# Optimization experiments

Measured on AMD Instinct MI355X. Metric: run time of the kernel, lower is better.

The kernel has to match this reference:

```python
import jax, jax.numpy as jnp
import numpy as np

BASE = 7.0
TWO_PI = 2.0 * np.pi
MAX_PATHS = 9

def _mod_phase(x):
    # ModularPhaseNorm(hidden, base=7): periodic phase nonlinearity
    return jnp.sin(TWO_PI * x / BASE)

def _branch(data, W):
    # data: [N, F, P], W: [O, F] -> [N, O, 3P] with per-path (neg, zero, pos) branches
    pos = jnp.einsum('nfp,of->nop', data, W)
    n, o, p = pos.shape
    tri = jnp.stack([-pos, jnp.zeros_like(pos), pos], axis=-1)  # [N,O,P,3]
    return tri.reshape(n, o, p * 3)

def _scorer(data, w1, b1, w2, b2):
    # data: [N, F, P] -> scores [N, P]  (linear -> modular phase -> linear)
    z = _mod_phase(jnp.einsum('nfp,hf->nph', data, w1) + b1)
    return (jnp.einsum('nph,oh->npo', z, w2) + b2)[..., 0]

def _prune(data, weights):
    # keep top-k paths by softmax weight, renormalize kept weights
    w_k, idx = jax.lax.top_k(weights, MAX_PATHS)
    data_k = jnp.take_along_axis(data, idx[:, None, :], axis=2)
    w_k = w_k / jnp.clip(jnp.sum(w_k, axis=1, keepdims=True), 1e-8)
    return data_k, w_k

def _forward(x, W1, W2, Wout, s1a_w, s1a_b, s1b_w, s1b_b, s2a_w, s2a_b, s2b_w, s2b_b, soa_w, soa_b, sob_w, sob_b):
    batch, choices, dims = x.shape
    data = x.reshape(batch * choices, dims)[:, :, None]  # 1 path
    weights = None
    for W, aw, ab, bw, bb in ((W1, s1a_w, s1a_b, s1b_w, s1b_b),
                              (W2, s2a_w, s2a_b, s2b_w, s2b_b)):
        data = jnp.tanh(_branch(data, W))
        weights = jax.nn.softmax(_scorer(data, aw, ab, bw, bb), axis=1)
        if data.shape[2] > MAX_PATHS:  # static shape condition
            data, weights = _prune(data, weights)
    data = _branch(data, Wout)  # [N, 1, 27]
    weights = jax.nn.softmax(_scorer(data, soa_w, soa_b, sob_w, sob_b), axis=1)
    if data.shape[2] > MAX_PATHS:
        data, weights = _prune(data, weights)
    out = jnp.sum(data * weights[:, None, :], axis=2)  # weighted collapse -> [N, 1]
    return out.reshape(batch, choices)

def setup_inputs():
    key = jax.random.key(0)
    ks = jax.random.split(key, 12)
    B, C, D, H, SH, SHO = 64, 64, 1024, 1024, 64, 32
    def lin(k, o, i):
        return jax.random.normal(k, (o, i), jnp.float32) / np.sqrt(i)
    return {
        'x': jax.random.normal(ks[0], (B, C, D), jnp.float32),
        'W1': lin(ks[1], H, D),
        'W2': lin(ks[2], H, H),
        'Wout': lin(ks[3], 1, H),
        's1a_w': lin(ks[4], SH, H), 's1a_b': jnp.zeros((SH,), jnp.float32),
        's1b_w': lin(ks[5], 1, SH), 's1b_b': jnp.zeros((1,), jnp.float32),
        's2a_w': lin(ks[6], SH, H), 's2a_b': jnp.zeros((SH,), jnp.float32),
        's2b_w': lin(ks[7], 1, SH), 's2b_b': jnp.zeros((1,), jnp.float32),
        'soa_w': lin(ks[8], SHO, 1), 'soa_b': jnp.zeros((SHO,), jnp.float32),
        'sob_w': lin(ks[9], 1, SHO), 'sob_b': jnp.zeros((1,), jnp.float32),
    }

def reference(x, W1, W2, Wout, s1a_w, s1a_b, s1b_w, s1b_b, s2a_w, s2a_b, s2b_w, s2b_b, soa_w, soa_b, sob_w, sob_b):
    return _forward(x, W1, W2, Wout, s1a_w, s1a_b, s1b_w, s1b_b, s2a_w, s2a_b, s2b_w, s2b_b, soa_w, soa_b, sob_w, sob_b)
```

## Files before the change

kernel.cpp:

```cpp
#include <hip/hip_runtime.h>


typedef __attribute__((ext_vector_type(4))) float     f32x4;
typedef __attribute__((ext_vector_type(8))) _Float16  f16x8;

#define AS1 __attribute__((address_space(1)))
#define AS3 __attribute__((address_space(3)))
#define GLOAD16(gp, lp) \
    __builtin_amdgcn_global_load_lds((AS1 const void*)(gp), (AS3 void*)(lp), 16, 0, 0)

__global__ __launch_bounds__(256)
void pbcs_cvt(const float* __restrict__ x,  _Float16* __restrict__ xo,
              const float* __restrict__ w1, _Float16* __restrict__ w1o,
              const float* __restrict__ w2, _Float16* __restrict__ w2o)
{
    const int b = blockIdx.x;
    const float* src; _Float16* dst; int idx;
    if (b < 2048)      { src = x;  dst = xo;  idx = b * 256 + threadIdx.x; }
    else if (b < 2560) { src = w1; dst = w1o; idx = (b - 2048) * 256 + threadIdx.x; }
    else               { src = w2; dst = w2o; idx = (b - 2560) * 256 + threadIdx.x; }
    const float4 v0 = ((const float4*)src)[idx * 2];
    const float4 v1 = ((const float4*)src)[idx * 2 + 1];
    f16x8 h;
    h[0] = (_Float16)v0.x; h[1] = (_Float16)v0.y;
    h[2] = (_Float16)v0.z; h[3] = (_Float16)v0.w;
    h[4] = (_Float16)v1.x; h[5] = (_Float16)v1.y;
    h[6] = (_Float16)v1.z; h[7] = (_Float16)v1.w;
    ((f16x8*)dst)[idx] = h;
}

template<int EPI>
__global__ __launch_bounds__(256, 2)
void pbcs_gemm16(const _Float16* __restrict__ A, const _Float16* __restrict__ B,
                 _Float16* __restrict__ Cout, const float* __restrict__ wout,
                 float* __restrict__ s_part)
{
    __shared__ char smem[2][32768];

    const int tid  = threadIdx.x;
    const int lane = tid & 63;
    const int wid  = tid >> 6;
    const int wm   = wid >> 1;
    const int wn   = wid & 1;
    const int l15  = lane & 15;
    const int g    = lane >> 4;

    const int b  = blockIdx.x;
    const int bm = (b & 7) * 4 + ((b >> 3) & 3);
    const int bn = b >> 5;

    const char* aS[4]; const char* bS[4]; int aD[4], bD[4];
#pragma unroll
    for (int j = 0; j < 4; ++j) {
        const int c = wid * 4 + j;
        const int r = c * 8 + (lane >> 3), s = lane & 7;
        aS[j] = (const char*)A + (size_t)(bm * 128 + r) * 2048 + 16 * (s ^ (r & 7));
        aD[j] = c * 1024;
        bS[j] = (const char*)B + (size_t)(bn * 128 + r) * 2048 + 16 * (s ^ (r & 7));
        bD[j] = 16384 + c * 1024;
    }

    int aoff[4][2], boff[4][2];
#pragma unroll
    for (int f = 0; f < 4; ++f) {
        const int ra = wm * 64 + f * 16 + l15;
        const int rb = wn * 64 + f * 16 + l15;
#pragma unroll
        for (int kh = 0; kh < 2; ++kh) {
            aoff[f][kh] = ra * 128 + 16 * (((kh << 2) | g) ^ (ra & 7));
            boff[f][kh] = 16384 + rb * 128 + 16 * (((kh << 2) | g) ^ (rb & 7));
        }
    }

    f32x4 acc[4][4];
#pragma unroll
    for (int i = 0; i < 4; ++i)
#pragma unroll
        for (int j = 0; j < 4; ++j) acc[i][j] = (f32x4)0.f;

#define STAGE(buf, kt) do {                                      \
        const int _ko = (kt) * 128;                              \
        _Pragma("unroll")                                        \
        for (int _j = 0; _j < 4; ++_j) {                         \
            GLOAD16(aS[_j] + _ko, smem[buf] + aD[_j]);           \
            GLOAD16(bS[_j] + _ko, smem[buf] + bD[_j]);           \
        }                                                        \
    } while (0)

#define COMPUTE(buf) do {                                                        \
        _Pragma("unroll")                                                        \
        for (int _kh = 0; _kh < 2; ++_kh) {                                      \
            f16x8 _a[4], _b[4];                                                  \
            _Pragma("unroll")                                                    \
            for (int _f = 0; _f < 4; ++_f) {                                     \
                _a[_f] = *(const f16x8*)(smem[buf] + aoff[_f][_kh]);             \
                _b[_f] = *(const f16x8*)(smem[buf] + boff[_f][_kh]);             \
            }                                                                    \
            _Pragma("unroll")                                                    \
            for (int _mf = 0; _mf < 4; ++_mf)                                    \
            _Pragma("unroll")                                                    \
            for (int _nf = 0; _nf < 4; ++_nf)                                    \
                acc[_mf][_nf] = __builtin_amdgcn_mfma_f32_16x16x32_f16(          \
                    _a[_mf], _b[_nf], acc[_mf][_nf], 0, 0, 0);                   \
        }                                                                        \
    } while (0)

    STAGE(0, 0);
    STAGE(1, 1);
#pragma unroll 1
    for (int t = 0; t < 15; ++t) {
        asm volatile("s_waitcnt vmcnt(8)" ::: "memory");
        __builtin_amdgcn_s_barrier();
        __builtin_amdgcn_sched_barrier(0);
        COMPUTE(t & 1);
        asm volatile("s_waitcnt lgkmcnt(0)" ::: "memory");
        __builtin_amdgcn_sched_barrier(0);
        __builtin_amdgcn_s_barrier();
        if (t < 14) STAGE(t & 1, t + 2);
    }
    asm volatile("s_waitcnt vmcnt(0)" ::: "memory");
    __builtin_amdgcn_s_barrier();
    __builtin_amdgcn_sched_barrier(0);
    COMPUTE(1);

    if (EPI == 0) {
#pragma unroll
        for (int mf = 0; mf < 4; ++mf)
#pragma unroll
        for (int nf = 0; nf < 4; ++nf)
#pragma unroll
        for (int jj = 0; jj < 4; ++jj) {
            const int row = bm * 128 + wm * 64 + mf * 16 + g * 4 + jj;
            const int col = bn * 128 + wn * 64 + nf * 16 + l15;
            Cout[(size_t)row * 1024 + col] = (_Float16)tanhf(acc[mf][nf][jj]);
        }
    } else {
        float w[4];
#pragma unroll
        for (int nf = 0; nf < 4; ++nf)
            w[nf] = wout[bn * 128 + wn * 64 + nf * 16 + l15];
#pragma unroll
        for (int mf = 0; mf < 4; ++mf)
#pragma unroll
        for (int jj = 0; jj < 4; ++jj) {
            float v = 0.f;
#pragma unroll
            for (int nf = 0; nf < 4; ++nf)
                v += tanhf(acc[mf][nf][jj]) * w[nf];
            v += __shfl_xor(v, 1, 64);
            v += __shfl_xor(v, 2, 64);
            v += __shfl_xor(v, 4, 64);
            v += __shfl_xor(v, 8, 64);
            if (l15 == 0) {
                const int row = bm * 128 + wm * 64 + mf * 16 + g * 4 + jj;
                s_part[row * 16 + bn * 2 + wn] = v;
            }
        }
    }
#undef STAGE
#undef COMPUTE
}

__global__ __launch_bounds__(256)
void pbcs_finalize(const float* __restrict__ s_part,
                   const float* __restrict__ soa_w, const float* __restrict__ soa_b,
                   const float* __restrict__ sob_w, const float* __restrict__ sob_b,
                   float* __restrict__ out, int Nrows)
{
    const int row  = blockIdx.x * 4 + (threadIdx.x >> 6);
    const int lane = threadIdx.x & 63;
    if (row >= Nrows) return;

    float part = (lane < 16) ? s_part[row * 16 + lane] : 0.f;
#pragma unroll
    for (int off = 32; off > 0; off >>= 1) part += __shfl_xor(part, off, 64);
    const float s = part;

    const float C7 = 0.8975979010256552f;
    float tS = 0.f, tZ = 0.f, tN = 0.f;
    if (lane < 32) {
        const float aw = soa_w[lane];
        const float ab = soa_b[lane];
        const float bw = sob_w[lane];
        tS = bw * sinf(C7 * fmaf(aw,  s, ab));
        tZ = bw * sinf(C7 * ab);
        tN = bw * sinf(C7 * fmaf(aw, -s, ab));
    }
#pragma unroll
    for (int off = 32; off > 0; off >>= 1) {
        tS += __shfl_xor(tS, off, 64);
        tZ += __shfl_xor(tZ, off, 64);
        tN += __shfl_xor(tN, off, 64);
    }
    const float bb = sob_b[0];
    const float fS = tS + bb;
    const float f0 = tZ + bb;
    const float fN = tN + bb;

    const int j  = lane;
    const int kk = j / 3;
    const int q  = j - kk * 3;
    const int p  = ((0x101 >> kk) & 1) - ((0x044 >> kk) & 1);
    const int c  = (q == 0) ? -p : ((q == 2) ? p : 0);
    const float val = (float)c * s;
    const float sc  = (c == 0) ? f0 : ((c > 0) ? fS : fN);

    int rank = 0;
#pragma unroll 1
    for (int i = 0; i < 27; ++i) {
        const float sci = __shfl(sc, i, 64);
        rank += (sci > sc) || (sci == sc && i < j);
    }
    const float mx = fmaxf(fS, fmaxf(f0, fN));
    float e = (j < 27 && rank < 9) ? expf(sc - mx) : 0.f;
    float num = val * e;
    float den = e;
#pragma unroll
    for (int off = 32; off > 0; off >>= 1) {
        num += __shfl_xor(num, off, 64);
        den += __shfl_xor(den, off, 64);
    }
    if (lane == 0) out[row] = num / den;
}

extern "C" void kernel_launch(void* const* d_in, const int* in_sizes, int n_in,
                              void* d_out, int out_size, void* d_ws, size_t ws_size,
                              hipStream_t stream)
{
    const float* x     = (const float*)d_in[0];
    const float* W1    = (const float*)d_in[1];
    const float* W2    = (const float*)d_in[2];
    const float* Wout  = (const float*)d_in[3];
    const float* soa_w = (const float*)d_in[12];
    const float* soa_b = (const float*)d_in[13];
    const float* sob_w = (const float*)d_in[14];
    const float* sob_b = (const float*)d_in[15];

    const int Nr = 4096;
    char* ws = (char*)d_ws;
    _Float16* xf  = (_Float16*)ws;
    _Float16* t1f = (_Float16*)(ws + (8u  << 20));
    _Float16* w1f = (_Float16*)(ws + (16u << 20));
    _Float16* w2f = (_Float16*)(ws + (18u << 20));
    float* s_part = (float*)(ws + (20u << 20));

    pbcs_cvt<<<3072, 256, 0, stream>>>(x, xf, W1, w1f, W2, w2f);

    pbcs_gemm16<0><<<256, 256, 0, stream>>>(xf,  w1f, t1f, nullptr, nullptr);
    pbcs_gemm16<1><<<256, 256, 0, stream>>>(t1f, w2f, nullptr, Wout, s_part);

    pbcs_finalize<<<Nr / 4, 256, 0, stream>>>(s_part, soa_w, soa_b, sob_w, sob_b,
                                              (float*)d_out, Nr);
}
```

Measured before the change: 56.30 us.

## Retile GEMMs to 64x128 blocks of two waves with triple-buffered LDS

Changes the two fp16 MFMA GEMMs from 128x128 tiles with four waves to 64x128 tiles with two waves, doubling the grid to 512 blocks. Shared memory becomes a three-stage ring of 24KB buffers, and the wait allows more loads in flight. The block-to-tile mapping is also reworked so consecutive blocks spread across XCDs. The aim is to fill more CUs on the 256-CU part and hide more load latency, at the cost of less data reuse per block and more global/L2 traffic.

```diff
diff --git a/kernel.cpp b/kernel.cpp
--- a/kernel.cpp
+++ b/kernel.cpp
@@ -30,45 +30,51 @@
 }
 
 template<int EPI>
-__global__ __launch_bounds__(256, 2)
+__global__ __launch_bounds__(128)
 void pbcs_gemm16(const _Float16* __restrict__ A, const _Float16* __restrict__ B,
                  _Float16* __restrict__ Cout, const float* __restrict__ wout,
                  float* __restrict__ s_part)
 {
-    __shared__ char smem[2][32768];
+    __shared__ char smem[3][24576];
 
     const int tid  = threadIdx.x;
     const int lane = tid & 63;
     const int wid  = tid >> 6;
-    const int wm   = wid >> 1;
-    const int wn   = wid & 1;
     const int l15  = lane & 15;
     const int g    = lane >> 4;
 
     const int b  = blockIdx.x;
-    const int bm = (b & 7) * 4 + ((b >> 3) & 3);
-    const int bn = b >> 5;
-
-    const char* aS[4]; const char* bS[4]; int aD[4], bD[4];
-#pragma unroll
-    for (int j = 0; j < 4; ++j) {
-        const int c = wid * 4 + j;
-        const int r = c * 8 + (lane >> 3), s = lane & 7;
-        aS[j] = (const char*)A + (size_t)(bm * 128 + r) * 2048 + 16 * (s ^ (r & 7));
-        aD[j] = c * 1024;
-        bS[j] = (const char*)B + (size_t)(bn * 128 + r) * 2048 + 16 * (s ^ (r & 7));
-        bD[j] = 16384 + c * 1024;
-    }
+    const int id = (b & 7) * 64 + (b >> 3);
+    const int bm = id >> 3;
+    const int bn = id & 7;
+
+    const int r = lane >> 3, s = lane & 7;
+    const char* aBase = (const char*)A
+        + (size_t)(bm * 64 + wid * 8 + r) * 2048 + 16 * (s ^ r);
+    const char* bBase = (const char*)B
+        + (size_t)(bn * 128 + wid * 8 + r) * 2048 + 16 * (s ^ r);
+
+#define STAGE(buf, kt) do {                                                   \
+        const int _ko = (kt) * 128;                                           \
+        _Pragma("unroll")                                                     \
+        for (int _j = 0; _j < 4; ++_j)               \
+            GLOAD16(aBase + _j * (16 * 2048) + _ko,                           \
+                    smem[buf] + (2 * _j + wid) * 1024);                       \
+        _Pragma("unroll")                                                     \
+        for (int _j = 0; _j < 8; ++_j)               \
+            GLOAD16(bBase + _j * (16 * 2048) + _ko,                           \
+                    smem[buf] + 8192 + (2 * _j + wid) * 1024);                \
+    } while (0)
 
     int aoff[4][2], boff[4][2];
 #pragma unroll
     for (int f = 0; f < 4; ++f) {
-        const int ra = wm * 64 + f * 16 + l15;
-        const int rb = wn * 64 + f * 16 + l15;
+        const int ra = f * 16 + l15;
+        const int rb = wid * 64 + f * 16 + l15;
 #pragma unroll
         for (int kh = 0; kh < 2; ++kh) {
             aoff[f][kh] = ra * 128 + 16 * (((kh << 2) | g) ^ (ra & 7));
-            boff[f][kh] = 16384 + rb * 128 + 16 * (((kh << 2) | g) ^ (rb & 7));
+            boff[f][kh] = 8192 + rb * 128 + 16 * (((kh << 2) | g) ^ (rb & 7));
         }
     }
 
@@ -77,15 +83,6 @@
     for (int i = 0; i < 4; ++i)
 #pragma unroll
         for (int j = 0; j < 4; ++j) acc[i][j] = (f32x4)0.f;
-
-#define STAGE(buf, kt) do {                                      \
-        const int _ko = (kt) * 128;                              \
-        _Pragma("unroll")                                        \
-        for (int _j = 0; _j < 4; ++_j) {                         \
-            GLOAD16(aS[_j] + _ko, smem[buf] + aD[_j]);           \
-            GLOAD16(bS[_j] + _ko, smem[buf] + bD[_j]);           \
-        }                                                        \
-    } while (0)
 
 #define COMPUTE(buf) do {                                                        \
         _Pragma("unroll")                                                        \
@@ -107,21 +104,24 @@
 
     STAGE(0, 0);
     STAGE(1, 1);
+    int cb = 0, sb = 2;
 #pragma unroll 1
     for (int t = 0; t < 15; ++t) {
-        asm volatile("s_waitcnt vmcnt(8)" ::: "memory");
+        asm volatile("s_waitcnt vmcnt(12)" ::: "memory");
         __builtin_amdgcn_s_barrier();
         __builtin_amdgcn_sched_barrier(0);
-        COMPUTE(t & 1);
+        COMPUTE(cb);
         asm volatile("s_waitcnt lgkmcnt(0)" ::: "memory");
         __builtin_amdgcn_sched_barrier(0);
         __builtin_amdgcn_s_barrier();
-        if (t < 14) STAGE(t & 1, t + 2);
+        if (t < 14) STAGE(sb, t + 2);
+        cb = (cb == 2) ? 0 : cb + 1;
+        sb = (sb == 2) ? 0 : sb + 1;
     }
     asm volatile("s_waitcnt vmcnt(0)" ::: "memory");
     __builtin_amdgcn_s_barrier();
     __builtin_amdgcn_sched_barrier(0);
-    COMPUTE(1);
+    COMPUTE(0);
 
     if (EPI == 0) {
 #pragma unroll
@@ -130,15 +130,15 @@
         for (int nf = 0; nf < 4; ++nf)
 #pragma unroll
         for (int jj = 0; jj < 4; ++jj) {
-            const int row = bm * 128 + wm * 64 + mf * 16 + g * 4 + jj;
-            const int col = bn * 128 + wn * 64 + nf * 16 + l15;
+            const int row = bm * 64 + mf * 16 + g * 4 + jj;
+            const int col = bn * 128 + wid * 64 + nf * 16 + l15;
             Cout[(size_t)row * 1024 + col] = (_Float16)tanhf(acc[mf][nf][jj]);
         }
     } else {
         float w[4];
 #pragma unroll
         for (int nf = 0; nf < 4; ++nf)
-            w[nf] = wout[bn * 128 + wn * 64 + nf * 16 + l15];
+            w[nf] = wout[bn * 128 + wid * 64 + nf * 16 + l15];
 #pragma unroll
         for (int mf = 0; mf < 4; ++mf)
 #pragma unroll
@@ -152,8 +152,8 @@
             v += __shfl_xor(v, 4, 64);
             v += __shfl_xor(v, 8, 64);
             if (l15 == 0) {
-                const int row = bm * 128 + wm * 64 + mf * 16 + g * 4 + jj;
-                s_part[row * 16 + bn * 2 + wn] = v;
+                const int row = bm * 64 + mf * 16 + g * 4 + jj;
+                s_part[row * 16 + bn * 2 + wid] = v;
             }
         }
     }
@@ -246,8 +246,8 @@
 
     pbcs_cvt<<<3072, 256, 0, stream>>>(x, xf, W1, w1f, W2, w2f);
 
-    pbcs_gemm16<0><<<256, 256, 0, stream>>>(xf,  w1f, t1f, nullptr, nullptr);
-    pbcs_gemm16<1><<<256, 256, 0, stream>>>(t1f, w2f, nullptr, Wout, s_part);
+    pbcs_gemm16<0><<<512, 128, 0, stream>>>(xf,  w1f, t1f, nullptr, nullptr);
+    pbcs_gemm16<1><<<512, 128, 0, stream>>>(t1f, w2f, nullptr, Wout, s_part);
 
     pbcs_finalize<<<Nr / 4, 256, 0, stream>>>(s_part, soa_w, soa_b, sob_w, sob_b,
                                               (float*)d_out, Nr);
```

New measurement: 66.54 us. 1.18x slower.

## Split GEMM K dimension across two wave groups with LDS reduction

Applied to the files above, without the earlier changes.

Doubles the GEMM block to 512 threads, where two groups of four waves each handle half of the K range, with 128KB of dynamic LDS. Each group stages and computes its own K half in 8 iterations instead of 16, and the partial accumulators are then summed through LDS before the epilogue. The aim is more waves in flight per CU and a shorter serial K loop for the 256-block grid, which likely leaves CUs underfilled. In exchange it adds an LDS round-trip for the reduction, needs more LDS per block, and drops to one block per CU.

```diff
diff --git a/kernel.cpp b/kernel.cpp
--- a/kernel.cpp
+++ b/kernel.cpp
@@ -30,17 +30,18 @@
 }
 
 template<int EPI>
-__global__ __launch_bounds__(256, 2)
+__global__ __launch_bounds__(512, 1)
 void pbcs_gemm16(const _Float16* __restrict__ A, const _Float16* __restrict__ B,
                  _Float16* __restrict__ Cout, const float* __restrict__ wout,
                  float* __restrict__ s_part)
 {
-    __shared__ char smem[2][32768];
+    extern __shared__ char smem[];
 
     const int tid  = threadIdx.x;
     const int lane = tid & 63;
     const int wid  = tid >> 6;
-    const int wm   = wid >> 1;
+    const int wk   = wid >> 2;
+    const int wm   = (wid >> 1) & 1;
     const int wn   = wid & 1;
     const int l15  = lane & 15;
     const int g    = lane >> 4;
@@ -49,16 +50,25 @@
     const int bm = (b & 7) * 4 + ((b >> 3) & 3);
     const int bn = b >> 5;
 
-    const char* aS[4]; const char* bS[4]; int aD[4], bD[4];
-#pragma unroll
-    for (int j = 0; j < 4; ++j) {
-        const int c = wid * 4 + j;
-        const int r = c * 8 + (lane >> 3), s = lane & 7;
-        aS[j] = (const char*)A + (size_t)(bm * 128 + r) * 2048 + 16 * (s ^ (r & 7));
-        aD[j] = c * 1024;
-        bS[j] = (const char*)B + (size_t)(bn * 128 + r) * 2048 + 16 * (s ^ (r & 7));
-        bD[j] = 16384 + c * 1024;
-    }
+    const int r = lane >> 3, sslot = lane & 7;
+    const int isB = (wid >> 1) & 1;
+    const char* stageSrc[8]; int stageDst[8];
+#pragma unroll
+    for (int j = 0; j < 8; ++j) {
+        const int cc  = (wid & 1) * 8 + j;
+        const int row = (isB ? bn : bm) * 128 + cc * 8 + r;
+        const char* base = (const char*)(isB ? B : A);
+        stageSrc[j] = base + (size_t)row * 2048 + wk * 1024 + 16 * (sslot ^ r);
+        stageDst[j] = wk * 32768 + isB * 16384 + cc * 1024;
+    }
+
+#define STAGE(buf, kt) do {                                              \
+        const int _ko = (kt) * 128;                                      \
+        _Pragma("unroll")                                                \
+        for (int _j = 0; _j < 8; ++_j)                                   \
+            GLOAD16(stageSrc[_j] + _ko,                                  \
+                    smem + (buf) * 65536 + stageDst[_j]);                \
+    } while (0)
 
     int aoff[4][2], boff[4][2];
 #pragma unroll
@@ -78,23 +88,15 @@
 #pragma unroll
         for (int j = 0; j < 4; ++j) acc[i][j] = (f32x4)0.f;
 
-#define STAGE(buf, kt) do {                                      \
-        const int _ko = (kt) * 128;                              \
-        _Pragma("unroll")                                        \
-        for (int _j = 0; _j < 4; ++_j) {                         \
-            GLOAD16(aS[_j] + _ko, smem[buf] + aD[_j]);           \
-            GLOAD16(bS[_j] + _ko, smem[buf] + bD[_j]);           \
-        }                                                        \
-    } while (0)
-
 #define COMPUTE(buf) do {                                                        \
+        const char* _L = smem + (buf) * 65536 + wk * 32768;                      \
         _Pragma("unroll")                                                        \
         for (int _kh = 0; _kh < 2; ++_kh) {                                      \
             f16x8 _a[4], _b[4];                                                  \
             _Pragma("unroll")                                                    \
             for (int _f = 0; _f < 4; ++_f) {                                     \
-                _a[_f] = *(const f16x8*)(smem[buf] + aoff[_f][_kh]);             \
-                _b[_f] = *(const f16x8*)(smem[buf] + boff[_f][_kh]);             \
+                _a[_f] = *(const f16x8*)(_L + aoff[_f][_kh]);                    \
+                _b[_f] = *(const f16x8*)(_L + boff[_f][_kh]);                    \
             }                                                                    \
             _Pragma("unroll")                                                    \
             for (int _mf = 0; _mf < 4; ++_mf)                                    \
@@ -108,20 +110,36 @@
     STAGE(0, 0);
     STAGE(1, 1);
 #pragma unroll 1
-    for (int t = 0; t < 15; ++t) {
-        asm volatile("s_waitcnt vmcnt(8)" ::: "memory");
+    for (int t = 0; t < 8; ++t) {
+        if (t < 7) { asm volatile("s_waitcnt vmcnt(8)" ::: "memory"); }
+        else       { asm volatile("s_waitcnt vmcnt(0)" ::: "memory"); }
         __builtin_amdgcn_s_barrier();
         __builtin_amdgcn_sched_barrier(0);
         COMPUTE(t & 1);
         asm volatile("s_waitcnt lgkmcnt(0)" ::: "memory");
         __builtin_amdgcn_sched_barrier(0);
         __builtin_amdgcn_s_barrier();
-        if (t < 14) STAGE(t & 1, t + 2);
-    }
-    asm volatile("s_waitcnt vmcnt(0)" ::: "memory");
+        if (t < 6) STAGE(t & 1, t + 2);
+    }
+
+    const int pair = wm * 2 + wn;
+    if (wk == 1) {
+#pragma unroll
+        for (int mf = 0; mf < 4; ++mf)
+#pragma unroll
+        for (int nf = 0; nf < 4; ++nf)
+            *(f32x4*)(smem + pair * 16384 + (mf * 4 + nf) * 1024 + lane * 16)
+                = acc[mf][nf];
+    }
+    asm volatile("s_waitcnt lgkmcnt(0)" ::: "memory");
     __builtin_amdgcn_s_barrier();
-    __builtin_amdgcn_sched_barrier(0);
-    COMPUTE(1);
+    if (wk == 1) return;
+#pragma unroll
+    for (int mf = 0; mf < 4; ++mf)
+#pragma unroll
+    for (int nf = 0; nf < 4; ++nf)
+        acc[mf][nf] += *(const f32x4*)(smem + pair * 16384
+                                       + (mf * 4 + nf) * 1024 + lane * 16);
 
     if (EPI == 0) {
 #pragma unroll
@@ -244,10 +262,15 @@
     _Float16* w2f = (_Float16*)(ws + (18u << 20));
     float* s_part = (float*)(ws + (20u << 20));
 
+    hipFuncSetAttribute((const void*)pbcs_gemm16<0>,
+                        hipFuncAttributeMaxDynamicSharedMemorySize, 131072);
+    hipFuncSetAttribute((const void*)pbcs_gemm16<1>,
+                        hipFuncAttributeMaxDynamicSharedMemorySize, 131072);
+
     pbcs_cvt<<<3072, 256, 0, stream>>>(x, xf, W1, w1f, W2, w2f);
 
-    pbcs_gemm16<0><<<256, 256, 0, stream>>>(xf,  w1f, t1f, nullptr, nullptr);
-    pbcs_gemm16<1><<<256, 256, 0, stream>>>(t1f, w2f, nullptr, Wout, s_part);
+    pbcs_gemm16<0><<<256, 512, 131072, stream>>>(xf,  w1f, t1f, nullptr, nullptr);
+    pbcs_gemm16<1><<<256, 512, 131072, stream>>>(t1f, w2f, nullptr, Wout, s_part);
 
     pbcs_finalize<<<Nr / 4, 256, 0, stream>>>(s_part, soa_w, soa_b, sob_w, sob_b,
                                               (float*)d_out, Nr);
```

Result: no change. 56.63 us (+0.6%).

## Fuse fp32-to-fp16 conversion of x into first GEMM's LDS load path

Applied to the files above, without the earlier changes.

The separate pass that converted the 16 MB fp32 input x to fp16 is removed. The first GEMM now streams fp32 x tiles directly into LDS and converts to fp16 in registers before the MFMA. This drops a full read and write of x through global memory. In exchange it doubles A-tile LDS traffic and uses 96 KB of dynamic shared memory, which limits the GEMM to one block per CU, so latency hiding may suffer.

```diff
diff --git a/kernel.cpp b/kernel.cpp
--- a/kernel.cpp
+++ b/kernel.cpp
@@ -10,15 +10,13 @@
     __builtin_amdgcn_global_load_lds((AS1 const void*)(gp), (AS3 void*)(lp), 16, 0, 0)
 
 __global__ __launch_bounds__(256)
-void pbcs_cvt(const float* __restrict__ x,  _Float16* __restrict__ xo,
-              const float* __restrict__ w1, _Float16* __restrict__ w1o,
-              const float* __restrict__ w2, _Float16* __restrict__ w2o)
+void pbcs_cvt_w(const float* __restrict__ w1, _Float16* __restrict__ w1o,
+                const float* __restrict__ w2, _Float16* __restrict__ w2o)
 {
     const int b = blockIdx.x;
     const float* src; _Float16* dst; int idx;
-    if (b < 2048)      { src = x;  dst = xo;  idx = b * 256 + threadIdx.x; }
-    else if (b < 2560) { src = w1; dst = w1o; idx = (b - 2048) * 256 + threadIdx.x; }
-    else               { src = w2; dst = w2o; idx = (b - 2560) * 256 + threadIdx.x; }
+    if (b < 512) { src = w1; dst = w1o; idx = b * 256 + threadIdx.x; }
+    else         { src = w2; dst = w2o; idx = (b - 512) * 256 + threadIdx.x; }
     const float4 v0 = ((const float4*)src)[idx * 2];
     const float4 v1 = ((const float4*)src)[idx * 2 + 1];
     f16x8 h;
@@ -29,13 +27,11 @@
     ((f16x8*)dst)[idx] = h;
 }
 
-template<int EPI>
-__global__ __launch_bounds__(256, 2)
-void pbcs_gemm16(const _Float16* __restrict__ A, const _Float16* __restrict__ B,
-                 _Float16* __restrict__ Cout, const float* __restrict__ wout,
-                 float* __restrict__ s_part)
-{
-    __shared__ char smem[2][32768];
+__global__ __launch_bounds__(256, 1)
+void pbcs_gemm_xf32(const float* __restrict__ A, const _Float16* __restrict__ B,
+                    _Float16* __restrict__ Cout)
+{
+    extern __shared__ char smem[];
 
     const int tid  = threadIdx.x;
     const int lane = tid & 63;
@@ -44,6 +40,130 @@
     const int wn   = wid & 1;
     const int l15  = lane & 15;
     const int g    = lane >> 4;
+    const int m7   = l15 & 7;
+
+    const int b  = blockIdx.x;
+    const int bm = (b & 7) * 4 + ((b >> 3) & 3);
+    const int bn = b >> 5;
+
+    const int r = lane >> 3, s = lane & 7;
+    const char* aS[8]; int aD[8];
+#pragma unroll
+    for (int j = 0; j < 8; ++j) {
+        const int c    = wid * 8 + j;
+        const int row4 = c * 4 + (r >> 1);
+        const int kh   = r & 1;
+        aS[j] = (const char*)A + (size_t)(bm * 128 + row4) * 4096
+              + kh * 128 + 16 * (s ^ (row4 & 7));
+        aD[j] = c * 1024;
+    }
+    const char* bS[4]; int bD[4];
+#pragma unroll
+    for (int j = 0; j < 4; ++j) {
+        const int c  = wid * 4 + j;
+        const int rr = c * 8 + r;
+        bS[j] = (const char*)B + (size_t)(bn * 128 + rr) * 2048 + 16 * (s ^ (rr & 7));
+        bD[j] = 32768 + c * 1024;
+    }
+
+#define STAGE1(buf, kt) do {                                         \
+        char* _D = smem + (buf) * 49152;                             \
+        _Pragma("unroll")                                            \
+        for (int _j = 0; _j < 8; ++_j)                               \
+            GLOAD16(aS[_j] + (kt) * 256, _D + aD[_j]);               \
+        _Pragma("unroll")                                            \
+        for (int _j = 0; _j < 4; ++_j)                               \
+            GLOAD16(bS[_j] + (kt) * 128, _D + bD[_j]);               \
+    } while (0)
+
+    int aoff[4][2], boff[4][2];
+#pragma unroll
+    for (int f = 0; f < 4; ++f) {
+        const int arow = wm * 64 + f * 16 + l15;
+        const int brow = wn * 64 + f * 16 + l15;
+#pragma unroll
+        for (int kh = 0; kh < 2; ++kh) {
+            aoff[f][kh] = arow * 256 + kh * 128 + 16 * ((2 * g) ^ m7);
+            boff[f][kh] = 32768 + brow * 128 + 16 * (((kh << 2) | g) ^ (brow & 7));
+        }
+    }
+
+    f32x4 acc[4][4];
+#pragma unroll
+    for (int i = 0; i < 4; ++i)
+#pragma unroll
+        for (int j = 0; j < 4; ++j) acc[i][j] = (f32x4)0.f;
+
+#define COMPUTE1(buf) do {                                                       \
+        const char* _L = smem + (buf) * 49152;                                   \
+        _Pragma("unroll")                                                        \
+        for (int _kh = 0; _kh < 2; ++_kh) {                                      \
+            f16x8 _a[4], _b[4];                                                  \
+            _Pragma("unroll")                                                    \
+            for (int _f = 0; _f < 4; ++_f) {                                     \
+                const f32x4 _x0 = *(const f32x4*)(_L + aoff[_f][_kh]);           \
+                const f32x4 _x1 = *(const f32x4*)(_L + (aoff[_f][_kh] ^ 16));    \
+                _Pragma("unroll")                                                \
+                for (int _e = 0; _e < 4; ++_e) {                                 \
+                    _a[_f][_e]     = (_Float16)_x0[_e];                          \
+                    _a[_f][_e + 4] = (_Float16)_x1[_e];                          \
+                }                                                                \
+                _b[_f] = *(const f16x8*)(_L + boff[_f][_kh]);                    \
+            }                                                                    \
+            _Pragma("unroll")                                                    \
+            for (int _mf = 0; _mf < 4; ++_mf)                                    \
+            _Pragma("unroll")                                                    \
+            for (int _nf = 0; _nf < 4; ++_nf)                                    \
+                acc[_mf][_nf] = __builtin_amdgcn_mfma_f32_16x16x32_f16(          \
+                    _a[_mf], _b[_nf], acc[_mf][_nf], 0, 0, 0);                   \
+        }                                                                        \
+    } while (0)
+
+    STAGE1(0, 0);
+    STAGE1(1, 1);
+#pragma unroll 1
+    for (int t = 0; t < 15; ++t) {
+        asm volatile("s_waitcnt vmcnt(12)" ::: "memory");
+        __builtin_amdgcn_s_barrier();
+        __builtin_amdgcn_sched_barrier(0);
+        COMPUTE1(t & 1);
+        asm volatile("s_waitcnt lgkmcnt(0)" ::: "memory");
+        __builtin_amdgcn_sched_barrier(0);
+        __builtin_amdgcn_s_barrier();
+        if (t < 14) STAGE1(t & 1, t + 2);
+    }
+    asm volatile("s_waitcnt vmcnt(0)" ::: "memory");
+    __builtin_amdgcn_s_barrier();
+    __builtin_amdgcn_sched_barrier(0);
+    COMPUTE1(1);
+
+#pragma unroll
+    for (int mf = 0; mf < 4; ++mf)
+#pragma unroll
+    for (int nf = 0; nf < 4; ++nf)
+#pragma unroll
+    for (int jj = 0; jj < 4; ++jj) {
+        const int row = bm * 128 + wm * 64 + mf * 16 + g * 4 + jj;
+        const int col = bn * 128 + wn * 64 + nf * 16 + l15;
+        Cout[(size_t)row * 1024 + col] = (_Float16)tanhf(acc[mf][nf][jj]);
+    }
+#undef STAGE1
+#undef COMPUTE1
+}
+
+__global__ __launch_bounds__(256, 2)
+void pbcs_gemm2(const _Float16* __restrict__ A, const _Float16* __restrict__ B,
+                const float* __restrict__ wout, float* __restrict__ s_part)
+{
+    __shared__ char smem[2][32768];
+
+    const int tid  = threadIdx.x;
+    const int lane = tid & 63;
+    const int wid  = tid >> 6;
+    const int wm   = wid >> 1;
+    const int wn   = wid & 1;
+    const int l15  = lane & 15;
+    const int g    = lane >> 4;
 
     const int b  = blockIdx.x;
     const int bm = (b & 7) * 4 + ((b >> 3) & 3);
@@ -78,7 +198,7 @@
 #pragma unroll
         for (int j = 0; j < 4; ++j) acc[i][j] = (f32x4)0.f;
 
-#define STAGE(buf, kt) do {                                      \
+#define STAGE2(buf, kt) do {                                     \
         const int _ko = (kt) * 128;                              \
         _Pragma("unroll")                                        \
         for (int _j = 0; _j < 4; ++_j) {                         \
@@ -87,7 +207,7 @@
         }                                                        \
     } while (0)
 
-#define COMPUTE(buf) do {                                                        \
+#define COMPUTE2(buf) do {                                                       \
         _Pragma("unroll")                                                        \
         for (int _kh = 0; _kh < 2; ++_kh) {                                      \
             f16x8 _a[4], _b[4];                                                  \
@@ -105,60 +225,47 @@
         }                                                                        \
     } while (0)
 
-    STAGE(0, 0);
-    STAGE(1, 1);
+    STAGE2(0, 0);
+    STAGE2(1, 1);
 #pragma unroll 1
     for (int t = 0; t < 15; ++t) {
         asm volatile("s_waitcnt vmcnt(8)" ::: "memory");
         __builtin_amdgcn_s_barrier();
         __builtin_amdgcn_sched_barrier(0);
-        COMPUTE(t & 1);
+        COMPUTE2(t & 1);
         asm volatile("s_waitcnt lgkmcnt(0)" ::: "memory");
         __builtin_amdgcn_sched_barrier(0);
         __builtin_amdgcn_s_barrier();
-        if (t < 14) STAGE(t & 1, t + 2);
+        if (t < 14) STAGE2(t & 1, t + 2);
     }
     asm volatile("s_waitcnt vmcnt(0)" ::: "memory");
     __builtin_amdgcn_s_barrier();
     __builtin_amdgcn_sched_barrier(0);
-    COMPUTE(1);
-
-    if (EPI == 0) {
-#pragma unroll
-        for (int mf = 0; mf < 4; ++mf)
+    COMPUTE2(1);
+
+    float w[4];
+#pragma unroll
+    for (int nf = 0; nf < 4; ++nf)
+        w[nf] = wout[bn * 128 + wn * 64 + nf * 16 + l15];
+#pragma unroll
+    for (int mf = 0; mf < 4; ++mf)
+#pragma unroll
+    for (int jj = 0; jj < 4; ++jj) {
+        float v = 0.f;
 #pragma unroll
         for (int nf = 0; nf < 4; ++nf)
-#pragma unroll
-        for (int jj = 0; jj < 4; ++jj) {
+            v += tanhf(acc[mf][nf][jj]) * w[nf];
+        v += __shfl_xor(v, 1, 64);
+        v += __shfl_xor(v, 2, 64);
+        v += __shfl_xor(v, 4, 64);
+        v += __shfl_xor(v, 8, 64);
+        if (l15 == 0) {
             const int row = bm * 128 + wm * 64 + mf * 16 + g * 4 + jj;
-            const int col = bn * 128 + wn * 64 + nf * 16 + l15;
-            Cout[(size_t)row * 1024 + col] = (_Float16)tanhf(acc[mf][nf][jj]);
+            s_part[row * 16 + bn * 2 + wn] = v;
         }
-    } else {
-        float w[4];
-#pragma unroll
-        for (int nf = 0; nf < 4; ++nf)
-            w[nf] = wout[bn * 128 + wn * 64 + nf * 16 + l15];
-#pragma unroll
-        for (int mf = 0; mf < 4; ++mf)
-#pragma unroll
-        for (int jj = 0; jj < 4; ++jj) {
-            float v = 0.f;
-#pragma unroll
-            for (int nf = 0; nf < 4; ++nf)
-                v += tanhf(acc[mf][nf][jj]) * w[nf];
-            v += __shfl_xor(v, 1, 64);
-            v += __shfl_xor(v, 2, 64);
-            v += __shfl_xor(v, 4, 64);
-            v += __shfl_xor(v, 8, 64);
-            if (l15 == 0) {
-                const int row = bm * 128 + wm * 64 + mf * 16 + g * 4 + jj;
-                s_part[row * 16 + bn * 2 + wn] = v;
-            }
-        }
-    }
-#undef STAGE
-#undef COMPUTE
+    }
+#undef STAGE2
+#undef COMPUTE2
 }
 
 __global__ __launch_bounds__(256)
@@ -238,16 +345,18 @@
 
     const int Nr = 4096;
     char* ws = (char*)d_ws;
-    _Float16* xf  = (_Float16*)ws;
-    _Float16* t1f = (_Float16*)(ws + (8u  << 20));
-    _Float16* w1f = (_Float16*)(ws + (16u << 20));
-    _Float16* w2f = (_Float16*)(ws + (18u << 20));
-    float* s_part = (float*)(ws + (20u << 20));
-
-    pbcs_cvt<<<3072, 256, 0, stream>>>(x, xf, W1, w1f, W2, w2f);
-
-    pbcs_gemm16<0><<<256, 256, 0, stream>>>(xf,  w1f, t1f, nullptr, nullptr);
-    pbcs_gemm16<1><<<256, 256, 0, stream>>>(t1f, w2f, nullptr, Wout, s_part);
+    _Float16* t1f = (_Float16*)ws;
+    _Float16* w1f = (_Float16*)(ws + (8u  << 20));
+    _Float16* w2f = (_Float16*)(ws + (10u << 20));
+    float* s_part = (float*)(ws + (12u << 20));
+
+    hipFuncSetAttribute((const void*)pbcs_gemm_xf32,
+                        hipFuncAttributeMaxDynamicSharedMemorySize, 98304);
+
+    pbcs_cvt_w<<<1024, 256, 0, stream>>>(W1, w1f, W2, w2f);
+
+    pbcs_gemm_xf32<<<256, 256, 98304, stream>>>(x, w1f, t1f);
+    pbcs_gemm2<<<256, 256, 0, stream>>>(t1f, w2f, Wout, s_part);
 
     pbcs_finalize<<<Nr / 4, 256, 0, stream>>>(s_part, soa_w, soa_b, sob_w, sob_b,
                                               (float*)d_out, Nr);
```

Measured after the change: 59.46 us. 5.6% more time.
